# Kernel tuning notes

Measured on AMD Instinct MI355X. Metric: run time of the kernel, lower is better.

## Reference

```python
import jax, jax.numpy as jnp
import numpy as np
from jax import lax

H = W = 4096

def _directional_filters():
    f0   = [[0,0,0],[0,1,-1],[0,0,0]]
    f45  = [[0,0,0],[0,1,0],[0,0,-1]]
    f90  = [[0,0,0],[0,1,0],[0,-1,0]]
    f135 = [[0,0,0],[0,1,0],[-1,0,0]]
    f180 = [[0,0,0],[-1,1,0],[0,0,0]]
    f225 = [[-1,0,0],[0,1,0],[0,0,0]]
    f270 = [[0,-1,0],[0,1,0],[0,0,0]]
    f315 = [[0,0,-1],[0,1,0],[0,0,0]]
    w = np.stack([f0,f45,f90,f135,f180,f225,f270,f315]).astype(np.float32)
    return jnp.asarray(w[:, None, :, :])  # [8,1,3,3]

def setup_inputs() -> dict:
    key = jax.random.key(0)
    k1, k2 = jax.random.split(key)
    grad_magnitude = jax.random.uniform(k1, (1, 1, H, W), dtype=jnp.float32)
    # orientation in degrees, quantized to multiples of 45 as in Canny
    grad_orientation = jax.random.randint(k2, (1, 1, H, W), 0, 8).astype(jnp.float32) * 45.0
    weight = _directional_filters()
    bias = jnp.zeros((8,), dtype=jnp.float32)
    return {"grad_magnitude": grad_magnitude, "grad_orientation": grad_orientation,
            "weight": weight, "bias": bias}

def reference(grad_magnitude, grad_orientation, weight, bias):
    # directional 3x3 conv, 1 -> 8 channels, 'SAME' padding
    all_filtered = lax.conv_general_dilated(
        grad_magnitude, weight, window_strides=(1, 1), padding='SAME')
    all_filtered = all_filtered + bias[None, :, None, None]  # [1,8,H,W]
    # per-pixel orientation channel indices (floor matches torch .long())
    idx_pos = jnp.floor(grad_orientation / 45.0).astype(jnp.int32) % 8  # [1,1,H,W]
    idx_neg = (idx_pos + 4) % 8
    f = all_filtered[0]                                  # [8,H,W]
    pos = jnp.take_along_axis(f, idx_pos[0], axis=0)     # [1,H,W]
    neg = jnp.take_along_axis(f, idx_neg[0], axis=0)     # [1,H,W]
    is_max = jnp.minimum(pos, neg) > 0.0                 # [1,H,W]
    thin_edges = jnp.where(is_max[None], grad_magnitude, 0.0)  # [1,1,H,W]
    return thin_edges
```

## Files before the change

### kernel.cpp

```cpp
#include <hip/hip_runtime.h>


constexpr int H = 4096;
constexpr int W = 4096;

typedef float v4f __attribute__((ext_vector_type(4)));

__device__ __forceinline__ v4f nms_row(const float u6[6], const float c6[6],
                                       const float d6[6], v4f m4, v4f o4,
                                       const float b[8])
{
    v4f res;
    const float m[4] = {m4.x, m4.y, m4.z, m4.w};
    const float o[4] = {o4.x, o4.y, o4.z, o4.w};
    float r[4];
    #pragma unroll
    for (int k = 0; k < 4; ++k) {
        const int c = (int)(o[k] * 0.0222222222f + 0.5f);
        const bool b0 = (c & 1), b1 = (c & 2), b2 = (c & 4);

        const float t0 = c6[k + 2] - b[0];
        const float t1 = d6[k + 2] - b[1];
        const float t2 = d6[k + 1] - b[2];
        const float t3 = d6[k]     - b[3];
        const float t4 = c6[k]     - b[4];
        const float t5 = u6[k]     - b[5];
        const float t6 = u6[k + 1] - b[6];
        const float t7 = u6[k + 2] - b[7];

        const float s01 = b0 ? t1 : t0;
        const float s23 = b0 ? t3 : t2;
        const float s45 = b0 ? t5 : t4;
        const float s67 = b0 ? t7 : t6;
        const float lo  = b1 ? s23 : s01;
        const float hi  = b1 ? s67 : s45;
        const float tp  = b2 ? hi : lo;
        const float tn  = b2 ? lo : hi;

        r[k] = (m[k] > fmaxf(tp, tn)) ? m[k] : 0.0f;
    }
    res.x = r[0]; res.y = r[1]; res.z = r[2]; res.w = r[3];
    return res;
}

__global__ __launch_bounds__(256) void nms_kernel(
    const float* __restrict__ mag,
    const float* __restrict__ orient,
    const float* __restrict__ bias,
    float* __restrict__ out)
{
    const int tid  = blockIdx.x * blockDim.x + threadIdx.x;
    const int lane = threadIdx.x & 63;
    const int ty   = tid >> 10;
    const int xq   = tid & 1023;
    const int x0   = xq << 2;
    const int y0   = ty << 1;
    const long base0 = ((long)y0 << 12) + x0;
    const long base1 = base0 + W;

    const bool has_up = (y0 > 0);
    const bool has_dn = (y0 + 2 < H);
    const v4f r0 = *reinterpret_cast<const v4f*>(mag + base0);
    const v4f r1 = *reinterpret_cast<const v4f*>(mag + base1);
    v4f uu = {0.f, 0.f, 0.f, 0.f};
    v4f dd = {0.f, 0.f, 0.f, 0.f};
    if (has_up) uu = *reinterpret_cast<const v4f*>(mag + base0 - W);
    if (has_dn) dd = *reinterpret_cast<const v4f*>(mag + base1 + W);

    const v4f o0 = __builtin_nontemporal_load(reinterpret_cast<const v4f*>(orient + base0));
    const v4f o1 = __builtin_nontemporal_load(reinterpret_cast<const v4f*>(orient + base1));

    float lU = __shfl_up(uu.w, 1), l0 = __shfl_up(r0.w, 1),
          l1 = __shfl_up(r1.w, 1), lD = __shfl_up(dd.w, 1);
    float rU = __shfl_down(uu.x, 1), q0 = __shfl_down(r0.x, 1),
          q1 = __shfl_down(r1.x, 1), rD = __shfl_down(dd.x, 1);
    if (lane == 0) {
        lU = l0 = l1 = lD = 0.f;
        if (x0 > 0) {
            l0 = mag[base0 - 1];
            l1 = mag[base1 - 1];
            if (has_up) lU = mag[base0 - W - 1];
            if (has_dn) lD = mag[base1 + W - 1];
        }
    }
    if (lane == 63) {
        rU = q0 = q1 = rD = 0.f;
        if (x0 + 4 < W) {
            q0 = mag[base0 + 4];
            q1 = mag[base1 + 4];
            if (has_up) rU = mag[base0 - W + 4];
            if (has_dn) rD = mag[base1 + W + 4];
        }
    }

    const float U6[6] = {lU, uu.x, uu.y, uu.z, uu.w, rU};
    const float C0[6] = {l0, r0.x, r0.y, r0.z, r0.w, q0};
    const float C1[6] = {l1, r1.x, r1.y, r1.z, r1.w, q1};
    const float D6[6] = {lD, dd.x, dd.y, dd.z, dd.w, rD};

    float b[8];
    #pragma unroll
    for (int i = 0; i < 8; ++i) b[i] = bias[i];

    const v4f res0 = nms_row(U6, C0, C1, r0, o0, b);
    const v4f res1 = nms_row(C0, C1, D6, r1, o1, b);

    __builtin_nontemporal_store(res0, reinterpret_cast<v4f*>(out + base0));
    __builtin_nontemporal_store(res1, reinterpret_cast<v4f*>(out + base1));
}

extern "C" void kernel_launch(void* const* d_in, const int* in_sizes, int n_in,
                              void* d_out, int out_size, void* d_ws, size_t ws_size,
                              hipStream_t stream) {
    const float* mag    = (const float*)d_in[0];
    const float* orient = (const float*)d_in[1];
    const float* bias   = (const float*)d_in[3];
    float* out = (float*)d_out;

    const int total = (H / 2) * (W / 4);
    dim3 block(256);
    dim3 grid(total / 256);
    hipLaunchKernelGGL(nms_kernel, grid, block, 0, stream,
                       mag, orient, bias, out);
}
```

Before: 166.9 us.

## Process four rows per thread and remap blocks to XCD-local row strips

Each thread now computes a 4x4 output tile instead of 2x4, loading six magnitude rows, so halo reads per output row drop from 2 to 1.5 loads. Block indices are remapped so consecutive blocks on the same XCD (bid&7) cover adjacent horizontal strips, which should improve L2 locality for the overlapping halo rows. Out-of-range halo rows are clamped to valid addresses and zeroed by multiplication instead of being branched around. The trade-off is higher register pressure and half as many threads.

```diff
diff --git a/kernel.cpp b/kernel.cpp
--- a/kernel.cpp
+++ b/kernel.cpp
@@ -49,64 +49,88 @@
     const float* __restrict__ bias,
     float* __restrict__ out)
 {
-    const int tid  = blockIdx.x * blockDim.x + threadIdx.x;
-    const int lane = threadIdx.x & 63;
-    const int ty   = tid >> 10;
-    const int xq   = tid & 1023;
-    const int x0   = xq << 2;
-    const int y0   = ty << 1;
-    const long base0 = ((long)y0 << 12) + x0;
-    const long base1 = base0 + W;
+    const int bid   = blockIdx.x;
+    const int xcd   = bid & 7;
+    const int j     = bid >> 3;
+    const int sband = j >> 2;
+    const int bq    = j & 3;
+    const int strip = xcd * 128 + sband;
+    const int lane  = threadIdx.x & 63;
 
-    const bool has_up = (y0 > 0);
-    const bool has_dn = (y0 + 2 < H);
-    const v4f r0 = *reinterpret_cast<const v4f*>(mag + base0);
-    const v4f r1 = *reinterpret_cast<const v4f*>(mag + base1);
-    v4f uu = {0.f, 0.f, 0.f, 0.f};
-    v4f dd = {0.f, 0.f, 0.f, 0.f};
-    if (has_up) uu = *reinterpret_cast<const v4f*>(mag + base0 - W);
-    if (has_dn) dd = *reinterpret_cast<const v4f*>(mag + base1 + W);
+    const int xq = bq * 256 + threadIdx.x;
+    const int x0 = xq << 2;
+    const int y0 = strip << 2;
 
-    const v4f o0 = __builtin_nontemporal_load(reinterpret_cast<const v4f*>(orient + base0));
-    const v4f o1 = __builtin_nontemporal_load(reinterpret_cast<const v4f*>(orient + base1));
+    const long rbase = ((long)y0 << 12) + x0;
 
-    float lU = __shfl_up(uu.w, 1), l0 = __shfl_up(r0.w, 1),
-          l1 = __shfl_up(r1.w, 1), lD = __shfl_up(dd.w, 1);
-    float rU = __shfl_down(uu.x, 1), q0 = __shfl_down(r0.x, 1),
-          q1 = __shfl_down(r1.x, 1), rD = __shfl_down(dd.x, 1);
-    if (lane == 0) {
-        lU = l0 = l1 = lD = 0.f;
-        if (x0 > 0) {
-            l0 = mag[base0 - 1];
-            l1 = mag[base1 - 1];
-            if (has_up) lU = mag[base0 - W - 1];
-            if (has_dn) lD = mag[base1 + W - 1];
-        }
-    }
-    if (lane == 63) {
-        rU = q0 = q1 = rD = 0.f;
-        if (x0 + 4 < W) {
-            q0 = mag[base0 + 4];
-            q1 = mag[base1 + 4];
-            if (has_up) rU = mag[base0 - W + 4];
-            if (has_dn) rD = mag[base1 + W + 4];
-        }
-    }
+    const float mtop = (y0 > 0)     ? 1.f : 0.f;
+    const float mbot = (y0 + 4 < H) ? 1.f : 0.f;
+    const long off[6] = {
+        (y0 > 0) ? -(long)W : 0L,
+        0L, (long)W, 2L * W, 3L * W,
+        (y0 + 4 < H) ? 4L * W : 3L * W
+    };
 
-    const float U6[6] = {lU, uu.x, uu.y, uu.z, uu.w, rU};
-    const float C0[6] = {l0, r0.x, r0.y, r0.z, r0.w, q0};
-    const float C1[6] = {l1, r1.x, r1.y, r1.z, r1.w, q1};
-    const float D6[6] = {lD, dd.x, dd.y, dd.z, dd.w, rD};
+    v4f rr[6];
+    #pragma unroll
+    for (int i = 0; i < 6; ++i)
+        rr[i] = *reinterpret_cast<const v4f*>(mag + rbase + off[i]);
+
+    v4f oo[4];
+    #pragma unroll
+    for (int i = 0; i < 4; ++i)
+        oo[i] = __builtin_nontemporal_load(
+            reinterpret_cast<const v4f*>(orient + rbase + (long)i * W));
 
     float b[8];
     #pragma unroll
     for (int i = 0; i < 8; ++i) b[i] = bias[i];
 
-    const v4f res0 = nms_row(U6, C0, C1, r0, o0, b);
-    const v4f res1 = nms_row(C0, C1, D6, r1, o1, b);
+    rr[0] *= mtop;
+    rr[5] *= mbot;
 
-    __builtin_nontemporal_store(res0, reinterpret_cast<v4f*>(out + base0));
-    __builtin_nontemporal_store(res1, reinterpret_cast<v4f*>(out + base1));
+    float lf[6], rt[6];
+    #pragma unroll
+    for (int i = 0; i < 6; ++i) {
+        lf[i] = __shfl_up(rr[i].w, 1);
+        rt[i] = __shfl_down(rr[i].x, 1);
+    }
+    if (lane == 0) {
+        #pragma unroll
+        for (int i = 0; i < 6; ++i) lf[i] = 0.f;
+        if (x0 > 0) {
+            #pragma unroll
+            for (int i = 0; i < 6; ++i) lf[i] = mag[rbase + off[i] - 1];
+            lf[0] *= mtop;
+            lf[5] *= mbot;
+        }
+    }
+    if (lane == 63) {
+        #pragma unroll
+        for (int i = 0; i < 6; ++i) rt[i] = 0.f;
+        if (x0 + 4 < W) {
+            #pragma unroll
+            for (int i = 0; i < 6; ++i) rt[i] = mag[rbase + off[i] + 4];
+            rt[0] *= mtop;
+            rt[5] *= mbot;
+        }
+    }
+
+    float R[6][6];
+    #pragma unroll
+    for (int i = 0; i < 6; ++i) {
+        R[i][0] = lf[i];
+        R[i][1] = rr[i].x; R[i][2] = rr[i].y;
+        R[i][3] = rr[i].z; R[i][4] = rr[i].w;
+        R[i][5] = rt[i];
+    }
+
+    #pragma unroll
+    for (int jr = 0; jr < 4; ++jr) {
+        const v4f res = nms_row(R[jr], R[jr + 1], R[jr + 2], rr[jr + 1], oo[jr], b);
+        __builtin_nontemporal_store(
+            res, reinterpret_cast<v4f*>(out + rbase + (long)jr * W));
+    }
 }
 
 extern "C" void kernel_launch(void* const* d_in, const int* in_sizes, int n_in,
@@ -117,7 +141,7 @@
     const float* bias   = (const float*)d_in[3];
     float* out = (float*)d_out;
 
-    const int total = (H / 2) * (W / 4);
+    const int total = (H / 4) * (W / 4);
     dim3 block(256);
     dim3 grid(total / 256);
     hipLaunchKernelGGL(nms_kernel, grid, block, 0, stream,
```

After: 171.4 us. 1.03x slower.

## Process strided row strips per thread with software-prefetched tiles

Applied to the files above, without the earlier changes.

Each thread now walks 8 rows spaced 512 apart, one row per iteration. The next tile's loads are issued before the current tile is computed and stored, to overlap memory latency with work. The previous layout shared two adjacent rows per thread. Now every row reloads its own up and down neighbours, which adds redundant mag reads, and orient loads no longer use nontemporal hints.

```diff
diff --git a/kernel.cpp b/kernel.cpp
--- a/kernel.cpp
+++ b/kernel.cpp
@@ -3,8 +3,44 @@
 
 constexpr int H = 4096;
 constexpr int W = 4096;
+constexpr int T = 8;
+constexpr int ROWSTEP = 512;
 
 typedef float v4f __attribute__((ext_vector_type(4)));
+
+struct Tile {
+    v4f u, c, d, o;
+    float lfu, lfc, lfd, rtu, rtc, rtd;
+    float mtop, mbot;
+};
+
+__device__ __forceinline__ Tile load_tile(const float* __restrict__ mag,
+                                          const float* __restrict__ orient,
+                                          long base, int y, int x0, int lane)
+{
+    Tile t;
+    const long uo = (y > 0)     ? -(long)W : 0;
+    const long dn = (y < H - 1) ?  (long)W : 0;
+    t.c = *reinterpret_cast<const v4f*>(mag + base);
+    t.u = *reinterpret_cast<const v4f*>(mag + base + uo);
+    t.d = *reinterpret_cast<const v4f*>(mag + base + dn);
+    t.o = *reinterpret_cast<const v4f*>(orient + base);
+    t.mtop = (y > 0)     ? 1.f : 0.f;
+    t.mbot = (y < H - 1) ? 1.f : 0.f;
+    t.lfu = t.lfc = t.lfd = 0.f;
+    t.rtu = t.rtc = t.rtd = 0.f;
+    if (lane == 0 && x0 > 0) {
+        t.lfc = mag[base - 1];
+        t.lfu = mag[base + uo - 1];
+        t.lfd = mag[base + dn - 1];
+    }
+    if (lane == 63 && x0 + 4 < W) {
+        t.rtc = mag[base + 4];
+        t.rtu = mag[base + uo + 4];
+        t.rtd = mag[base + dn + 4];
+    }
+    return t;
+}
 
 __device__ __forceinline__ v4f nms_row(const float u6[6], const float c6[6],
                                        const float d6[6], v4f m4, v4f o4,
@@ -43,70 +79,52 @@
     return res;
 }
 
+__device__ __forceinline__ void process(const Tile& t, const float b[8],
+                                        float* __restrict__ out, long base,
+                                        int lane)
+{
+    const v4f u = t.u * t.mtop;
+    const v4f d = t.d * t.mbot;
+    float lu = __shfl_up(u.w, 1), lc = __shfl_up(t.c.w, 1), ld2 = __shfl_up(d.w, 1);
+    float ru = __shfl_down(u.x, 1), rc = __shfl_down(t.c.x, 1), rd = __shfl_down(d.x, 1);
+    if (lane == 0)  { lu = t.lfu * t.mtop; lc = t.lfc; ld2 = t.lfd * t.mbot; }
+    if (lane == 63) { ru = t.rtu * t.mtop; rc = t.rtc; rd  = t.rtd * t.mbot; }
+
+    const float u6[6] = {lu,  u.x,   u.y,   u.z,   u.w,   ru};
+    const float c6[6] = {lc,  t.c.x, t.c.y, t.c.z, t.c.w, rc};
+    const float d6[6] = {ld2, d.x,   d.y,   d.z,   d.w,   rd};
+
+    const v4f res = nms_row(u6, c6, d6, t.c, t.o, b);
+    __builtin_nontemporal_store(res, reinterpret_cast<v4f*>(out + base));
+}
+
 __global__ __launch_bounds__(256) void nms_kernel(
     const float* __restrict__ mag,
     const float* __restrict__ orient,
     const float* __restrict__ bias,
     float* __restrict__ out)
 {
-    const int tid  = blockIdx.x * blockDim.x + threadIdx.x;
+    const int tid  = blockIdx.x * 256 + threadIdx.x;
     const int lane = threadIdx.x & 63;
-    const int ty   = tid >> 10;
-    const int xq   = tid & 1023;
-    const int x0   = xq << 2;
-    const int y0   = ty << 1;
+    const int y0   = tid >> 10;
+    const int x0   = (tid & 1023) << 2;
     const long base0 = ((long)y0 << 12) + x0;
-    const long base1 = base0 + W;
-
-    const bool has_up = (y0 > 0);
-    const bool has_dn = (y0 + 2 < H);
-    const v4f r0 = *reinterpret_cast<const v4f*>(mag + base0);
-    const v4f r1 = *reinterpret_cast<const v4f*>(mag + base1);
-    v4f uu = {0.f, 0.f, 0.f, 0.f};
-    v4f dd = {0.f, 0.f, 0.f, 0.f};
-    if (has_up) uu = *reinterpret_cast<const v4f*>(mag + base0 - W);
-    if (has_dn) dd = *reinterpret_cast<const v4f*>(mag + base1 + W);
-
-    const v4f o0 = __builtin_nontemporal_load(reinterpret_cast<const v4f*>(orient + base0));
-    const v4f o1 = __builtin_nontemporal_load(reinterpret_cast<const v4f*>(orient + base1));
-
-    float lU = __shfl_up(uu.w, 1), l0 = __shfl_up(r0.w, 1),
-          l1 = __shfl_up(r1.w, 1), lD = __shfl_up(dd.w, 1);
-    float rU = __shfl_down(uu.x, 1), q0 = __shfl_down(r0.x, 1),
-          q1 = __shfl_down(r1.x, 1), rD = __shfl_down(dd.x, 1);
-    if (lane == 0) {
-        lU = l0 = l1 = lD = 0.f;
-        if (x0 > 0) {
-            l0 = mag[base0 - 1];
-            l1 = mag[base1 - 1];
-            if (has_up) lU = mag[base0 - W - 1];
-            if (has_dn) lD = mag[base1 + W - 1];
-        }
-    }
-    if (lane == 63) {
-        rU = q0 = q1 = rD = 0.f;
-        if (x0 + 4 < W) {
-            q0 = mag[base0 + 4];
-            q1 = mag[base1 + 4];
-            if (has_up) rU = mag[base0 - W + 4];
-            if (has_dn) rD = mag[base1 + W + 4];
-        }
-    }
-
-    const float U6[6] = {lU, uu.x, uu.y, uu.z, uu.w, rU};
-    const float C0[6] = {l0, r0.x, r0.y, r0.z, r0.w, q0};
-    const float C1[6] = {l1, r1.x, r1.y, r1.z, r1.w, q1};
-    const float D6[6] = {lD, dd.x, dd.y, dd.z, dd.w, rD};
+    const long bstep = (long)ROWSTEP * W;
 
     float b[8];
     #pragma unroll
     for (int i = 0; i < 8; ++i) b[i] = bias[i];
 
-    const v4f res0 = nms_row(U6, C0, C1, r0, o0, b);
-    const v4f res1 = nms_row(C0, C1, D6, r1, o1, b);
-
-    __builtin_nontemporal_store(res0, reinterpret_cast<v4f*>(out + base0));
-    __builtin_nontemporal_store(res1, reinterpret_cast<v4f*>(out + base1));
+    Tile cur = load_tile(mag, orient, base0, y0, x0, lane);
+    long pbase = base0;
+    for (int it = 1; it < T; ++it) {
+        const long nbase = base0 + (long)it * bstep;
+        Tile nxt = load_tile(mag, orient, nbase, y0 + it * ROWSTEP, x0, lane);
+        process(cur, b, out, pbase, lane);
+        cur = nxt;
+        pbase = nbase;
+    }
+    process(cur, b, out, pbase, lane);
 }
 
 extern "C" void kernel_launch(void* const* d_in, const int* in_sizes, int n_in,
@@ -117,9 +135,9 @@
     const float* bias   = (const float*)d_in[3];
     float* out = (float*)d_out;
 
-    const int total = (H / 2) * (W / 4);
+    const int total_threads = (H / ROWSTEP == T) ? (H * W / 4 / T) : (H * W / 4 / T);
     dim3 block(256);
-    dim3 grid(total / 256);
+    dim3 grid(total_threads / 256);
     hipLaunchKernelGGL(nms_kernel, grid, block, 0, stream,
                        mag, orient, bias, out);
 }
```

Result: slower. 178.4 us (+6.8%).
